# Kernel tuning notes

Hardware: AMD Instinct MI355X
Metric: run time of the kernel (lower is better)

The kernel has to match this reference:

```python
import jax, jax.numpy as jnp
import numpy as np
from jax import lax

T_STEPS = 4
TAU = 2.0
V_THRESHOLD = 1.0
V_RESET = 0.0
ATAN_ALPHA = 2.0

@jax.custom_vjp
def atan_spike(x):
    # Heaviside forward, ATan surrogate gradient (spikingjelly surrogate.ATan, alpha=2)
    return (x >= 0.0).astype(x.dtype)

def _atan_fwd(x):
    return atan_spike(x), x

def _atan_bwd(x, g):
    grad = (ATAN_ALPHA / 2.0) / (1.0 + (jnp.pi / 2.0 * ATAN_ALPHA * x) ** 2)
    return (g * grad,)

atan_spike.defvjp(_atan_fwd, _atan_bwd)

def setup_inputs() -> dict:
    key = jax.random.key(0)
    inputs = jax.random.normal(key, (32, 720, 862), dtype=jnp.float32)  # B, L, C
    return {"inputs": inputs}

def reference(inputs) -> jnp.ndarray:
    # repeat along a new leading time dim: (T, B, L, C)
    x = jnp.broadcast_to(inputs[None], (T_STEPS,) + inputs.shape)
    # permute(0,1,3,2) -> (T, B, C, L)
    x = jnp.transpose(x, (0, 1, 3, 2))

    def step(v, xt):
        # LIF with decay_input=True (spikingjelly default):
        # v <- v + (x - (v - v_reset)) / tau
        v = v + (xt - (v - V_RESET)) / TAU
        s = atan_spike(v - V_THRESHOLD)
        sd = lax.stop_gradient(s)  # detach_reset=True
        v = (1.0 - sd) * v + sd * V_RESET  # hard reset
        return v, s

    v0 = jnp.zeros_like(x[0])
    _, spks = lax.scan(step, v0, x)
    return spks  # (T, B, C, L)
```

## Files before the change

### kernel.cpp

```cpp
#include <hip/hip_runtime.h>


#define B_DIM 32
#define L_DIM 720
#define C_DIM 862
#define T_STEPS 4
#define TILE 32

__global__ __launch_bounds__(256)
void lif_repeat_encoder(const float* __restrict__ in, float* __restrict__ out) {
    __shared__ float tile[TILE][TILE + 1];

    const int b  = blockIdx.z;
    const int l0 = blockIdx.x * TILE;
    const int c0 = blockIdx.y * TILE;
    const int tx = threadIdx.x;
    const int ty = threadIdx.y;

    const float* __restrict__ inb = in + (size_t)b * L_DIM * C_DIM;

    {
        const int c = c0 + tx;
        if (c < C_DIM) {
#pragma unroll
            for (int k = 0; k < 4; ++k) {
                const int l = l0 + ty + 8 * k;
                if (l < L_DIM) {
                    tile[ty + 8 * k][tx] = inb[(size_t)l * C_DIM + c];
                }
            }
        }
    }
    __syncthreads();

    const int l = l0 + tx;
    if (l >= L_DIM) return;

    const size_t plane = (size_t)B_DIM * C_DIM * L_DIM;

#pragma unroll
    for (int k = 0; k < 4; ++k) {
        const int c = c0 + ty + 8 * k;
        if (c >= C_DIM) continue;

        const float x = tile[tx][ty + 8 * k];

        float v = 0.0f;
        float s[T_STEPS];
#pragma unroll
        for (int t = 0; t < T_STEPS; ++t) {
            v = v + (x - v) * 0.5f;
            const float sp = (v - 1.0f >= 0.0f) ? 1.0f : 0.0f;
            s[t] = sp;
            v = (sp != 0.0f) ? 0.0f : v;
        }

        const size_t base = ((size_t)b * C_DIM + c) * L_DIM + l;
#pragma unroll
        for (int t = 0; t < T_STEPS; ++t) {
            out[(size_t)t * plane + base] = s[t];
        }
    }
}

extern "C" void kernel_launch(void* const* d_in, const int* in_sizes, int n_in,
                              void* d_out, int out_size, void* d_ws, size_t ws_size,
                              hipStream_t stream) {
    const float* in = (const float*)d_in[0];
    float* out = (float*)d_out;

    dim3 block(32, 8, 1);
    dim3 grid((L_DIM + TILE - 1) / TILE,
              (C_DIM + TILE - 1) / TILE,
              B_DIM);

    lif_repeat_encoder<<<grid, block, 0, stream>>>(in, out);
}
```

Baseline: 393.9 us.

## Use 64x64 tiles with vectorized loads and nontemporal float4 stores

Enlarges the transpose tile to 64x64 and gives each thread four contiguous elements. Input is read as float2 pairs and output is written as float4 nontemporal stores. The aim is fewer, wider memory transactions for this bandwidth-bound transpose and spike encoder, and less cache pollution from the large output. The cost is more shared memory per block and possible bank conflicts on the strided shared-memory writes. L_DIM of 720 is not a multiple of 64, so the last L tile is partially empty.

```diff
diff --git a/kernel.cpp b/kernel.cpp
--- a/kernel.cpp
+++ b/kernel.cpp
@@ -5,60 +5,94 @@
 #define L_DIM 720
 #define C_DIM 862
 #define T_STEPS 4
-#define TILE 32
+#define TL 64
+#define TC 64
+#define LROW 68
+
+typedef float v2f __attribute__((ext_vector_type(2)));
+typedef float v4f __attribute__((ext_vector_type(4)));
 
 __global__ __launch_bounds__(256)
 void lif_repeat_encoder(const float* __restrict__ in, float* __restrict__ out) {
-    __shared__ float tile[TILE][TILE + 1];
+    __shared__ float smem[TC * LROW];
 
-    const int b  = blockIdx.z;
-    const int l0 = blockIdx.x * TILE;
-    const int c0 = blockIdx.y * TILE;
-    const int tx = threadIdx.x;
-    const int ty = threadIdx.y;
+    const int b   = blockIdx.z;
+    const int l0  = blockIdx.x * TL;
+    const int c0  = blockIdx.y * TC;
+    const int tid = threadIdx.x;
 
-    const float* __restrict__ inb = in + (size_t)b * L_DIM * C_DIM;
+    const float* __restrict__ inb = in + (size_t)b * (L_DIM * C_DIM);
 
     {
-        const int c = c0 + tx;
-        if (c < C_DIM) {
+        const int c4   = (tid & 15) << 2;
+        const int lrow = tid >> 4;
 #pragma unroll
-            for (int k = 0; k < 4; ++k) {
-                const int l = l0 + ty + 8 * k;
-                if (l < L_DIM) {
-                    tile[ty + 8 * k][tx] = inb[(size_t)l * C_DIM + c];
+        for (int p = 0; p < 4; ++p) {
+            const int ll = lrow + p * 16;
+            const int l  = l0 + ll;
+            if (l < L_DIM) {
+                const int c = c0 + c4;
+                const float* src = inb + (size_t)l * C_DIM + c;
+                if (c + 3 < C_DIM) {
+                    const v2f a = *(const v2f*)(src);
+                    const v2f d = *(const v2f*)(src + 2);
+                    smem[(c4 + 0) * LROW + ll] = a.x;
+                    smem[(c4 + 1) * LROW + ll] = a.y;
+                    smem[(c4 + 2) * LROW + ll] = d.x;
+                    smem[(c4 + 3) * LROW + ll] = d.y;
+                } else {
+#pragma unroll
+                    for (int i = 0; i < 4; ++i) {
+                        if (c + i < C_DIM)
+                            smem[(c4 + i) * LROW + ll] = src[i];
+                    }
                 }
             }
         }
     }
     __syncthreads();
 
-    const int l = l0 + tx;
+    const int l4   = (tid & 15) << 2;
+    const int crow = tid >> 4;
+    const int l    = l0 + l4;
     if (l >= L_DIM) return;
 
     const size_t plane = (size_t)B_DIM * C_DIM * L_DIM;
 
 #pragma unroll
-    for (int k = 0; k < 4; ++k) {
-        const int c = c0 + ty + 8 * k;
+    for (int q = 0; q < 4; ++q) {
+        const int cl = crow + q * 16;
+        const int c  = c0 + cl;
         if (c >= C_DIM) continue;
 
-        const float x = tile[tx][ty + 8 * k];
+        const v4f x = *(const v4f*)(smem + cl * LROW + l4);
 
-        float v = 0.0f;
-        float s[T_STEPS];
+        float sx[T_STEPS], sy[T_STEPS], sz[T_STEPS], sw[T_STEPS];
+        {
+            float v0 = 0.f, v1 = 0.f, v2 = 0.f, v3 = 0.f;
 #pragma unroll
-        for (int t = 0; t < T_STEPS; ++t) {
-            v = v + (x - v) * 0.5f;
-            const float sp = (v - 1.0f >= 0.0f) ? 1.0f : 0.0f;
-            s[t] = sp;
-            v = (sp != 0.0f) ? 0.0f : v;
+            for (int t = 0; t < T_STEPS; ++t) {
+                v0 += (x.x - v0) * 0.5f;
+                v1 += (x.y - v1) * 0.5f;
+                v2 += (x.z - v2) * 0.5f;
+                v3 += (x.w - v3) * 0.5f;
+                sx[t] = (v0 >= 1.0f) ? 1.0f : 0.0f;
+                sy[t] = (v1 >= 1.0f) ? 1.0f : 0.0f;
+                sz[t] = (v2 >= 1.0f) ? 1.0f : 0.0f;
+                sw[t] = (v3 >= 1.0f) ? 1.0f : 0.0f;
+                v0 = (v0 >= 1.0f) ? 0.0f : v0;
+                v1 = (v1 >= 1.0f) ? 0.0f : v1;
+                v2 = (v2 >= 1.0f) ? 0.0f : v2;
+                v3 = (v3 >= 1.0f) ? 0.0f : v3;
+            }
         }
 
         const size_t base = ((size_t)b * C_DIM + c) * L_DIM + l;
 #pragma unroll
         for (int t = 0; t < T_STEPS; ++t) {
-            out[(size_t)t * plane + base] = s[t];
+            v4f o;
+            o.x = sx[t]; o.y = sy[t]; o.z = sz[t]; o.w = sw[t];
+            __builtin_nontemporal_store(o, (v4f*)(out + (size_t)t * plane + base));
         }
     }
 }
@@ -69,9 +103,9 @@
     const float* in = (const float*)d_in[0];
     float* out = (float*)d_out;
 
-    dim3 block(32, 8, 1);
-    dim3 grid((L_DIM + TILE - 1) / TILE,
-              (C_DIM + TILE - 1) / TILE,
+    dim3 block(256, 1, 1);
+    dim3 grid((L_DIM + TL - 1) / TL,
+              (C_DIM + TC - 1) / TC,
               B_DIM);
 
     lif_repeat_encoder<<<grid, block, 0, stream>>>(in, out);
```

New measurement: 379.4 us. -3.7%, faster.
